# Kernel tuning notes

Hardware: AMD Instinct MI355X
Metric: run time of the kernel (lower is better)

The kernel has to match this reference:

```python
import jax, jax.numpy as jnp
from jax import lax
import numpy as np


def setup_inputs() -> dict:
    key = jax.random.key(0)
    encode_image = jax.random.normal(key, (32, 3, 512, 512), dtype=jnp.float32)
    return {"encode_image": encode_image, "w": 5}


def _box_blur(x, w):
    # cv2.blur with ksize (w, w): normalized box filter, BORDER_REFLECT_101 padding.
    # Implemented as a separable depthwise convolution (two 1D average passes).
    B, C, H, W = x.shape
    p = w // 2  # w is odd -> symmetric padding, matches cv2 default anchor
    xp = jnp.pad(x, ((0, 0), (0, 0), (p, p), (p, p)), mode="reflect")  # REFLECT_101
    kh = jnp.full((C, 1, w, 1), 1.0 / w, dtype=x.dtype)  # vertical pass
    kw = jnp.full((C, 1, 1, w), 1.0 / w, dtype=x.dtype)  # horizontal pass
    dn = ("NCHW", "OIHW", "NCHW")
    y = lax.conv_general_dilated(xp, kh, (1, 1), "VALID",
                                 dimension_numbers=dn, feature_group_count=C)
    y = lax.conv_general_dilated(y, kw, (1, 1), "VALID",
                                 dimension_numbers=dn, feature_group_count=C)
    return y  # (B, C, H, W)


def reference(encode_image, w):
    # Faithful to Smooth.forward: replaces noise_and_cover[0] with the box-blurred
    # image; we return the blurred tensor (the only modified element).
    return _box_blur(encode_image, w)
```

## Files before the change

kernel.cpp:

```cpp
#include <hip/hip_runtime.h>


#define IMG_H 512
#define IMG_W 512
#define NF4   (IMG_W / 4)
#define STRIP 32
#define NSTRIPS (IMG_H / STRIP)

struct F4 { float x, y, z, w; };
struct Raw { float4 b; float2 a, c; };

__global__ __launch_bounds__(128) void smooth_box5_mlp(
    const float* __restrict__ in, float* __restrict__ out)
{
    const int c4 = threadIdx.x;
    const int r0 = blockIdx.x * STRIP;
    const size_t planeOff = (size_t)blockIdx.y * (IMG_H * IMG_W);
    const float* __restrict__ ip = in + planeOff;
    float*       __restrict__ op = out + planeOff;

    const int xb = c4 * 4;
    const bool left  = (c4 == 0);
    const bool right = (c4 == NF4 - 1);
    const int xa = left  ? 0          : xb - 2;
    const int xc = right ? IMG_W - 8  : xb + 4;

    auto load_raw = [&](int r) -> Raw {
        int ry = (r < 0) ? -r : r;
        ry = (ry >= IMG_H) ? (2 * IMG_H - 2 - ry) : ry;
        const float* row = ip + (size_t)ry * IMG_W;
        Raw q;
        q.b = *(const float4*)(row + xb);
        q.a = *(const float2*)(row + xa);
        q.c = *(const float2*)(row + xc);
        return q;
    };

    auto hcomp = [&](const Raw& q) -> F4 {
        const float a2 = left  ? q.b.z : q.a.x;
        const float a3 = left  ? q.b.y : q.a.y;
        const float c0 = right ? q.b.z : q.c.x;
        const float c1 = right ? q.b.y : q.c.y;
        const float s = q.b.x + q.b.y + q.b.z + q.b.w;
        F4 h;
        h.x = s - q.b.w + a2 + a3;
        h.y = s + a3;
        h.z = s + c0;
        h.w = s - q.b.x + c0 + c1;
        return h;
    };

    Raw p[5];
    #pragma unroll
    for (int k = 0; k < 5; ++k) p[k] = load_raw(r0 - 2 + k);

    F4 h[6];
    #pragma unroll
    for (int k = 0; k < 5; ++k) h[k] = hcomp(p[k]);

    F4 S;
    S.x = h[0].x + h[1].x + h[2].x + h[3].x + h[4].x;
    S.y = h[0].y + h[1].y + h[2].y + h[3].y + h[4].y;
    S.z = h[0].z + h[1].z + h[2].z + h[3].z + h[4].z;
    S.w = h[0].w + h[1].w + h[2].w + h[3].w + h[4].w;

    const float inv = 0.2f * 0.2f;
    float* orow = op + (size_t)r0 * IMG_W + xb;

    #pragma unroll
    for (int j = 0; j < 4; ++j) {
        const int nload = (j < 3) ? 8 : 7;
        Raw q[8];
        #pragma unroll
        for (int k = 0; k < 8; ++k) {
            if (k < nload) q[k] = load_raw(r0 + 8 * j + 3 + k);
        }
        #pragma unroll
        for (int i = 0; i < 8; ++i) {
            const int rr = 8 * j + i;
            float4 o;
            o.x = S.x * inv; o.y = S.y * inv; o.z = S.z * inv; o.w = S.w * inv;
            *(float4*)orow = o;
            orow += IMG_W;
            if (rr < STRIP - 1) {
                const int inew = (rr + 5) % 6;
                const int iold = rr % 6;
                h[inew] = hcomp(q[i]);
                S.x += h[inew].x - h[iold].x;
                S.y += h[inew].y - h[iold].y;
                S.z += h[inew].z - h[iold].z;
                S.w += h[inew].w - h[iold].w;
            }
        }
    }
}

extern "C" void kernel_launch(void* const* d_in, const int* in_sizes, int n_in,
                              void* d_out, int out_size, void* d_ws, size_t ws_size,
                              hipStream_t stream) {
    const float* img = (const float*)d_in[0];
    float* out = (float*)d_out;
    const int BC = 32 * 3;
    dim3 grid(NSTRIPS, BC);
    dim3 block(128);
    smooth_box5_mlp<<<grid, block, 0, stream>>>(img, out);
}
```

Measured before the change: 202.5 us.

## Replace strip sliding-window kernel with flat one-row-per-thread box blur

Each thread now computes a single output row of four pixels by loading its five neighbouring input rows directly, instead of sliding a running vertical sum down a 32-row strip. The grid becomes a flat 1D launch of 256-thread blocks covering all planes. This aims to increase parallelism and memory-level concurrency and to remove the serial dependency chain per thread. In exchange it issues about five times as many global loads per output row, relying on L1/L2 to absorb the vertical reuse.

```diff
diff --git a/kernel.cpp b/kernel.cpp
--- a/kernel.cpp
+++ b/kernel.cpp
@@ -4,95 +4,58 @@
 #define IMG_H 512
 #define IMG_W 512
 #define NF4   (IMG_W / 4)
-#define STRIP 32
-#define NSTRIPS (IMG_H / STRIP)
 
 struct F4 { float x, y, z, w; };
 struct Raw { float4 b; float2 a, c; };
 
-__global__ __launch_bounds__(128) void smooth_box5_mlp(
+__global__ __launch_bounds__(256) void smooth_box5_flat(
     const float* __restrict__ in, float* __restrict__ out)
 {
-    const int c4 = threadIdx.x;
-    const int r0 = blockIdx.x * STRIP;
-    const size_t planeOff = (size_t)blockIdx.y * (IMG_H * IMG_W);
+    const int tid   = blockIdx.x * 256 + threadIdx.x;
+    const int c4    = tid & (NF4 - 1);
+    const int y     = (tid >> 7) & (IMG_H - 1);
+    const int plane = tid >> 16;
+
+    const size_t planeOff = (size_t)plane * (IMG_H * IMG_W);
     const float* __restrict__ ip = in + planeOff;
-    float*       __restrict__ op = out + planeOff;
 
     const int xb = c4 * 4;
     const bool left  = (c4 == 0);
     const bool right = (c4 == NF4 - 1);
-    const int xa = left  ? 0          : xb - 2;
-    const int xc = right ? IMG_W - 8  : xb + 4;
+    const int xa = left  ? 0         : xb - 2;
+    const int xc = right ? IMG_W - 8 : xb + 4;
 
-    auto load_raw = [&](int r) -> Raw {
-        int ry = (r < 0) ? -r : r;
+    Raw p[5];
+    #pragma unroll
+    for (int k = 0; k < 5; ++k) {
+        int ry = y + k - 2;
+        ry = (ry < 0) ? -ry : ry;
         ry = (ry >= IMG_H) ? (2 * IMG_H - 2 - ry) : ry;
         const float* row = ip + (size_t)ry * IMG_W;
-        Raw q;
-        q.b = *(const float4*)(row + xb);
-        q.a = *(const float2*)(row + xa);
-        q.c = *(const float2*)(row + xc);
-        return q;
-    };
+        p[k].b = *(const float4*)(row + xb);
+        p[k].a = *(const float2*)(row + xa);
+        p[k].c = *(const float2*)(row + xc);
+    }
 
-    auto hcomp = [&](const Raw& q) -> F4 {
+    F4 S = {0.f, 0.f, 0.f, 0.f};
+    #pragma unroll
+    for (int k = 0; k < 5; ++k) {
+        const Raw& q = p[k];
         const float a2 = left  ? q.b.z : q.a.x;
         const float a3 = left  ? q.b.y : q.a.y;
         const float c0 = right ? q.b.z : q.c.x;
         const float c1 = right ? q.b.y : q.c.y;
         const float s = q.b.x + q.b.y + q.b.z + q.b.w;
-        F4 h;
-        h.x = s - q.b.w + a2 + a3;
-        h.y = s + a3;
-        h.z = s + c0;
-        h.w = s - q.b.x + c0 + c1;
-        return h;
-    };
-
-    Raw p[5];
-    #pragma unroll
-    for (int k = 0; k < 5; ++k) p[k] = load_raw(r0 - 2 + k);
-
-    F4 h[6];
-    #pragma unroll
-    for (int k = 0; k < 5; ++k) h[k] = hcomp(p[k]);
-
-    F4 S;
-    S.x = h[0].x + h[1].x + h[2].x + h[3].x + h[4].x;
-    S.y = h[0].y + h[1].y + h[2].y + h[3].y + h[4].y;
-    S.z = h[0].z + h[1].z + h[2].z + h[3].z + h[4].z;
-    S.w = h[0].w + h[1].w + h[2].w + h[3].w + h[4].w;
+        S.x += s - q.b.w + a2 + a3;
+        S.y += s + a3;
+        S.z += s + c0;
+        S.w += s - q.b.x + c0 + c1;
+    }
 
     const float inv = 0.2f * 0.2f;
-    float* orow = op + (size_t)r0 * IMG_W + xb;
-
-    #pragma unroll
-    for (int j = 0; j < 4; ++j) {
-        const int nload = (j < 3) ? 8 : 7;
-        Raw q[8];
-        #pragma unroll
-        for (int k = 0; k < 8; ++k) {
-            if (k < nload) q[k] = load_raw(r0 + 8 * j + 3 + k);
-        }
-        #pragma unroll
-        for (int i = 0; i < 8; ++i) {
-            const int rr = 8 * j + i;
-            float4 o;
-            o.x = S.x * inv; o.y = S.y * inv; o.z = S.z * inv; o.w = S.w * inv;
-            *(float4*)orow = o;
-            orow += IMG_W;
-            if (rr < STRIP - 1) {
-                const int inew = (rr + 5) % 6;
-                const int iold = rr % 6;
-                h[inew] = hcomp(q[i]);
-                S.x += h[inew].x - h[iold].x;
-                S.y += h[inew].y - h[iold].y;
-                S.z += h[inew].z - h[iold].z;
-                S.w += h[inew].w - h[iold].w;
-            }
-        }
-    }
+    float4 o;
+    o.x = S.x * inv; o.y = S.y * inv; o.z = S.z * inv; o.w = S.w * inv;
+    *(float4*)(out + planeOff + (size_t)y * IMG_W + xb) = o;
 }
 
 extern "C" void kernel_launch(void* const* d_in, const int* in_sizes, int n_in,
@@ -100,8 +63,8 @@
                               hipStream_t stream) {
     const float* img = (const float*)d_in[0];
     float* out = (float*)d_out;
-    const int BC = 32 * 3;
-    dim3 grid(NSTRIPS, BC);
-    dim3 block(128);
-    smooth_box5_mlp<<<grid, block, 0, stream>>>(img, out);
+    const int total = 96 * IMG_H * NF4;
+    dim3 grid(total / 256);
+    dim3 block(256);
+    smooth_box5_flat<<<grid, block, 0, stream>>>(img, out);
 }
```

Measured after the change: 206.9 us. 1.02x slower.
